# Optimization experiments

Measured on AMD Instinct MI355X. Metric: run time of the kernel, lower is better.

## Reference

```python
import jax, jax.numpy as jnp
import numpy as np

DIM = 768
HEADS = 12
HD = DIM // HEADS
L = 196
N = 128


def layernorm(x, g, b, eps=1e-5):
    x32 = x.astype(jnp.float32)
    mu = jnp.mean(x32, axis=-1, keepdims=True)
    var = jnp.mean(jnp.square(x32 - mu), axis=-1, keepdims=True)
    return ((x32 - mu) * jax.lax.rsqrt(var + eps) * g + b).astype(x.dtype)


def setup_inputs() -> dict:
    key = jax.random.key(0)
    ks = jax.random.split(key, 16)
    s_lin = 1.0 / np.sqrt(DIM)
    s_hd = 1.0 / np.sqrt(HD)
    return {
        "x": jax.random.normal(ks[0], (L, N, DIM), jnp.float32),
        "cls": jax.random.normal(ks[1], (1, N, DIM), jnp.float32),
        "g1": jnp.ones((DIM,), jnp.float32),
        "b1": jnp.zeros((DIM,), jnp.float32),
        "g2": jnp.ones((DIM,), jnp.float32),
        "b2": jnp.zeros((DIM,), jnp.float32),
        "Wq": jax.random.uniform(ks[2], (DIM, DIM), jnp.float32, -s_lin, s_lin),
        "Wk": jax.random.uniform(ks[3], (DIM, DIM), jnp.float32, -s_lin, s_lin),
        "Wv": jax.random.uniform(ks[4], (DIM, DIM), jnp.float32, -s_lin, s_lin),
        "p1_w1": jax.random.uniform(ks[5], (HD, HD), jnp.float32, -s_hd, s_hd),
        "p1_b1": jax.random.uniform(ks[6], (HD,), jnp.float32, -s_hd, s_hd),
        "p1_w2": jax.random.uniform(ks[7], (HD, HD), jnp.float32, -s_hd, s_hd),
        "p1_b2": jax.random.uniform(ks[8], (HD,), jnp.float32, -s_hd, s_hd),
        "fc_w": jax.random.uniform(ks[9], (DIM, DIM), jnp.float32, -s_lin, s_lin),
        "fc_b": jax.random.uniform(ks[10], (DIM,), jnp.float32, -s_lin, s_lin),
        "proj_w": jax.random.uniform(ks[11], (DIM, DIM), jnp.float32, -s_lin, s_lin),
        "proj_b": jax.random.uniform(ks[12], (DIM,), jnp.float32, -s_lin, s_lin),
    }


def reference(x, cls, g1, b1, g2, b2, Wq, Wk, Wv, p1_w1, p1_b1, p1_w2, p1_b2, fc_w, fc_b, proj_w, proj_b):
    scale = HD ** (-0.5)
    xx = layernorm(jnp.concatenate([cls, x], axis=0), g1, b1)  # [L+1, N, D]
    q0 = xx[:1]   # [1, N, D] (residual)
    kv = xx[1:]   # [L, N, D]
    # torch nn.Linear: y = x @ W.T; B=1 hard-wired, keys flattened to L*N tokens
    q = (q0 @ Wq.T).reshape(1, N, HEADS, HD).transpose(0, 2, 1, 3)        # [1,H,N,hd]
    k = (kv @ Wk.T).reshape(1, L * N, HEADS, HD).transpose(0, 2, 1, 3)    # [1,H,LN,hd]
    v = (kv @ Wv.T).reshape(1, L * N, HEADS, HD).transpose(0, 2, 1, 3)    # [1,H,LN,hd]
    scores = jnp.einsum('bhqd,bhkd->bhqk', q, k) * scale                  # [1,H,N,LN]
    attn = jax.nn.softmax(scores, axis=-1)
    # predictor gate: MLP -> mean over head_dim -> softmax over singleton axis (=1)
    temq = jnp.tanh(jax.nn.relu(q @ p1_w1.T + p1_b1) @ p1_w2.T + p1_b2)   # [1,H,N,hd]
    temq = jnp.mean(temq, axis=-1, keepdims=True)                          # [1,H,N,1]
    temq = jax.nn.softmax(temq, axis=-1)                                   # ones (faithful)
    attn = (temq - 0.5) * attn
    ctx = jnp.einsum('bhqk,bhkd->bhqd', attn, v)                           # [1,H,N,hd]
    ctx = ctx.transpose(0, 2, 1, 3).reshape(1, N, DIM)
    q1 = q0 + ctx
    h = layernorm(q1, g2, b2)
    m = h @ fc_w.T + fc_b
    m = m * jax.nn.sigmoid(1.702 * m)  # QuickGELU
    m = m @ proj_w.T + proj_b
    return q1 + m  # [1, N, D]
```

## Files before the change

kernel.cpp:

```cpp
#include <hip/hip_runtime.h>

#define DIM 768
#define HEADS 12
#define HD 64
#define NB 128
#define ROWS_ALL 25216
#define ROWS_KV  25088
#define NCHUNK 64

typedef __attribute__((ext_vector_type(8))) short short8;
typedef __attribute__((ext_vector_type(4))) short short4v;
typedef __attribute__((ext_vector_type(4))) float f32x4;
typedef __attribute__((ext_vector_type(4))) unsigned int uint4v;

__device__ __forceinline__ unsigned short f2bf(float f) {
  union { float f; unsigned u; } a; a.f = f;
  return (unsigned short)((a.u + 0x7fffu + ((a.u >> 16) & 1u)) >> 16);
}
__device__ __forceinline__ float bf2f(unsigned short u) {
  union { unsigned u; float f; } a; a.u = ((unsigned)u) << 16;
  return a.f;
}

__device__ __forceinline__ void gload16(const void* g, void* l) {
  __builtin_amdgcn_global_load_lds(
      (__attribute__((address_space(1))) void*)g,
      (__attribute__((address_space(3))) void*)l, 16, 0, 0);
}

__global__ __launch_bounds__(256) void ln1_cast(
    const float* __restrict__ x, const float* __restrict__ cls,
    const float* __restrict__ g, const float* __restrict__ b,
    unsigned short* __restrict__ xx, float* __restrict__ q0f,
    const float* __restrict__ Wq, const float* __restrict__ Wk,
    const float* __restrict__ Wv, const float* __restrict__ fcw,
    const float* __restrict__ pw, unsigned short* __restrict__ wpk)
{
  int blk = blockIdx.x, tid = threadIdx.x;
  if (blk < ROWS_ALL / 4) {
    int row = blk * 4 + (tid >> 6);
    int lane = tid & 63;
    const float* src = (row < NB) ? (cls + (size_t)row * DIM)
                                  : (x + (size_t)(row - NB) * DIM);
    float4 v[3];
    float s = 0.f;
#pragma unroll
    for (int i = 0; i < 3; ++i) {
      v[i] = ((const float4*)src)[lane + 64 * i];
      s += v[i].x + v[i].y + v[i].z + v[i].w;
    }
#pragma unroll
    for (int o = 32; o; o >>= 1) s += __shfl_xor(s, o);
    float mean = s * (1.f / 768.f);
    float ss = 0.f;
#pragma unroll
    for (int i = 0; i < 3; ++i) {
      float a0 = v[i].x - mean, a1 = v[i].y - mean, a2 = v[i].z - mean, a3 = v[i].w - mean;
      ss += a0 * a0 + a1 * a1 + a2 * a2 + a3 * a3;
    }
#pragma unroll
    for (int o = 32; o; o >>= 1) ss += __shfl_xor(ss, o);
    float rs = rsqrtf(ss * (1.f / 768.f) + 1e-5f);
#pragma unroll
    for (int i = 0; i < 3; ++i) {
      int c4 = lane + 64 * i;
      float4 gv = ((const float4*)g)[c4];
      float4 bv = ((const float4*)b)[c4];
      float o0 = (v[i].x - mean) * rs * gv.x + bv.x;
      float o1 = (v[i].y - mean) * rs * gv.y + bv.y;
      float o2 = (v[i].z - mean) * rs * gv.z + bv.z;
      float o3 = (v[i].w - mean) * rs * gv.w + bv.w;
      ushort4 u; u.x = f2bf(o0); u.y = f2bf(o1); u.z = f2bf(o2); u.w = f2bf(o3);
      ((ushort4*)(xx + (size_t)row * DIM))[c4] = u;
      if (row < NB) {
        float4 fo; fo.x = o0; fo.y = o1; fo.z = o2; fo.w = o3;
        ((float4*)(q0f + (size_t)row * DIM))[c4] = fo;
      }
    }
  } else {
    int idx = blk - ROWS_ALL / 4;
    int w = idx / 576;
    int j4 = (idx % 576) * 256 + tid;
    const float* s = (w == 0) ? Wq : (w == 1) ? Wk : (w == 2) ? Wv
                   : (w == 3) ? fcw : pw;
    float4 v = ((const float4*)s)[j4];
    ushort4 u; u.x = f2bf(v.x); u.y = f2bf(v.y); u.z = f2bf(v.z); u.w = f2bf(v.w);
    ((ushort4*)(wpk + (size_t)w * (DIM * DIM)))[j4] = u;
  }
}

__global__ __launch_bounds__(256, 4) void gemm_fused(
    const unsigned short* __restrict__ xxkv, const unsigned short* __restrict__ Wkb,
    unsigned short* __restrict__ Kbf,
    const unsigned short* __restrict__ Wvb, unsigned short* __restrict__ Vtb,
    const unsigned short* __restrict__ xxall, const unsigned short* __restrict__ Wqb,
    unsigned short* __restrict__ Qbf)
{
  __shared__ unsigned short Asm[128 * 32];
  __shared__ unsigned short Bsm[128 * 32];
  int tid = threadIdx.x, wid = tid >> 6, lane = tid & 63;
  int l15 = lane & 15, l4 = lane >> 4;

  int nwg = gridDim.x;
  int bid = blockIdx.x;
  int q8 = nwg >> 3, r8 = nwg & 7;
  int xcd = bid & 7, rank = bid >> 3;
  int swz = (xcd < r8 ? xcd * (q8 + 1) : r8 * (q8 + 1) + (xcd - r8) * q8) + rank;

  const unsigned short *A, *Bt;
  unsigned short* C;
  int N, row0, col0;
  const int K = DIM;
  if (swz < 1176) {
    A = xxkv; Bt = Wkb; C = Kbf; N = DIM;
    row0 = (swz / 6) * 128; col0 = (swz % 6) * 128;
  } else if (swz < 2352) {
    int inner = swz - 1176;
    A = Wvb; Bt = xxkv; C = Vtb; N = ROWS_KV;
    row0 = (inner % 6) * 128; col0 = (inner / 6) * 128;
  } else {
    int inner = swz - 2352;
    A = xxall; Bt = Wqb; C = Qbf; N = DIM;
    row0 = 0; col0 = inner * 128;
  }

  int srow = tid >> 2;
  int sq = tid & 3;
  int sb = sq ^ ((srow >> 1) & 3);
  const char* Ag = (const char*)A + (size_t)(row0 + srow) * K * 2 + sb * 16;
  const char* Bg = (const char*)Bt + (size_t)(col0 + srow) * K * 2 + sb * 16;
  size_t rstep64 = (size_t)64 * K * 2;

  f32x4 acc[4][4] = {};
  int wr = (wid >> 1) * 64, wc = (wid & 1) * 64;
  const int nk = K >> 5;
  for (int t = 0; t < nk; ++t) {
    {
      const char* a0 = Ag + (size_t)t * 64;
      const char* b0 = Bg + (size_t)t * 64;
      char* la = (char*)Asm + wid * 1024;
      char* lb = (char*)Bsm + wid * 1024;
      gload16(a0,           la);
      gload16(a0 + rstep64, la + 4096);
      gload16(b0,           lb);
      gload16(b0 + rstep64, lb + 4096);
    }
    asm volatile("s_waitcnt vmcnt(0)" ::: "memory");
    __builtin_amdgcn_s_barrier();
    asm volatile("" ::: "memory");
    short8 aF[4], bF[4];
#pragma unroll
    for (int m = 0; m < 4; ++m) {
      int row = wr + m * 16 + l15;
      aF[m] = *(const short8*)((const char*)Asm + row * 64 + ((l4 ^ ((row >> 1) & 3)) << 4));
    }
#pragma unroll
    for (int n = 0; n < 4; ++n) {
      int row = wc + n * 16 + l15;
      bF[n] = *(const short8*)((const char*)Bsm + row * 64 + ((l4 ^ ((row >> 1) & 3)) << 4));
    }
    __builtin_amdgcn_s_setprio(1);
#pragma unroll
    for (int m = 0; m < 4; ++m)
#pragma unroll
      for (int n = 0; n < 4; ++n)
        acc[m][n] = __builtin_amdgcn_mfma_f32_16x16x32_bf16(aF[m], bF[n], acc[m][n], 0, 0, 0);
    __builtin_amdgcn_s_setprio(0);
    asm volatile("" ::: "memory");
    __builtin_amdgcn_s_barrier();
    asm volatile("" ::: "memory");
  }
#pragma unroll
  for (int m = 0; m < 4; ++m)
#pragma unroll
    for (int n = 0; n < 4; ++n)
#pragma unroll
      for (int r = 0; r < 4; ++r) {
        int rr = row0 + wr + m * 16 + l4 * 4 + r;
        int cc = col0 + wc + n * 16 + l15;
        C[(size_t)rr * N + cc] = f2bf(acc[m][n][r]);
      }
}

template <int EPI>
__global__ __launch_bounds__(256, 2) void gemm_bt64(
    const unsigned short* __restrict__ A, const unsigned short* __restrict__ Bt,
    void* __restrict__ Cout, int M, int N, int K,
    const float* __restrict__ bias, const float* __restrict__ addsrc)
{
  __shared__ unsigned short Asm[2][128 * 64];
  __shared__ unsigned short Bsm[2][128 * 64];
  int tid = threadIdx.x, wid = tid >> 6, lane = tid & 63;
  int l15 = lane & 15, l4 = lane >> 4;
  int row0 = blockIdx.y * 128, col0 = blockIdx.x * 128;

  int srow = tid >> 3;
  int scol = ((tid & 7) ^ (srow & 7)) << 4;
  const char* Ag = (const char*)A + (size_t)(row0 + srow) * K * 2 + scol;
  const char* Bg = (const char*)Bt + (size_t)(col0 + srow) * K * 2 + scol;
  size_t rstep32 = (size_t)32 * K * 2;

#define STAGE(buf, kt) do {                                           \
    const char* a0 = Ag + (size_t)(kt) * 128;                         \
    const char* b0 = Bg + (size_t)(kt) * 128;                         \
    char* la = (char*)Asm[buf] + wid * 1024;                          \
    char* lb = (char*)Bsm[buf] + wid * 1024;                          \
    gload16(a0,                la);                                   \
    gload16(a0 + rstep32,      la + 4096);                            \
    gload16(a0 + 2 * rstep32,  la + 8192);                            \
    gload16(a0 + 3 * rstep32,  la + 12288);                           \
    gload16(b0,                lb);                                   \
    gload16(b0 + rstep32,      lb + 4096);                            \
    gload16(b0 + 2 * rstep32,  lb + 8192);                            \
    gload16(b0 + 3 * rstep32,  lb + 12288);                           \
  } while (0)

  f32x4 acc[4][4] = {};
  int wr = (wid >> 1) * 64, wc = (wid & 1) * 64;
  int nk = K >> 6;
  STAGE(0, 0);
  for (int t = 0; t < nk; ++t) {
    int cur = t & 1;
    if (t + 1 < nk) {
      STAGE(cur ^ 1, t + 1);
      asm volatile("s_waitcnt vmcnt(8)" ::: "memory");
    } else {
      asm volatile("s_waitcnt vmcnt(0)" ::: "memory");
    }
    __builtin_amdgcn_s_barrier();
    asm volatile("" ::: "memory");
    const char* Ab = (const char*)Asm[cur];
    const char* Bb = (const char*)Bsm[cur];
#pragma unroll
    for (int kk = 0; kk < 2; ++kk) {
      short8 aF[4], bF[4];
#pragma unroll
      for (int m = 0; m < 4; ++m) {
        int row = wr + m * 16 + l15;
        aF[m] = *(const short8*)(Ab + row * 128 + ((((kk << 2) | l4) ^ (row & 7)) << 4));
      }
#pragma unroll
      for (int n = 0; n < 4; ++n) {
        int row = wc + n * 16 + l15;
        bF[n] = *(const short8*)(Bb + row * 128 + ((((kk << 2) | l4) ^ (row & 7)) << 4));
      }
#pragma unroll
      for (int m = 0; m < 4; ++m)
#pragma unroll
        for (int n = 0; n < 4; ++n)
          acc[m][n] = __builtin_amdgcn_mfma_f32_16x16x32_bf16(aF[m], bF[n], acc[m][n], 0, 0, 0);
    }
    asm volatile("" ::: "memory");
    __builtin_amdgcn_s_barrier();
    asm volatile("" ::: "memory");
  }
#undef STAGE
#pragma unroll
  for (int m = 0; m < 4; ++m)
#pragma unroll
    for (int n = 0; n < 4; ++n)
#pragma unroll
      for (int r = 0; r < 4; ++r) {
        int rr = row0 + wr + m * 16 + l4 * 4 + r;
        int cc = col0 + wc + n * 16 + l15;
        float v = acc[m][n][r];
        if (EPI == 1) {
          v += bias[cc];
          v = v / (1.f + __expf(-1.702f * v));
          ((unsigned short*)Cout)[(size_t)rr * N + cc] = f2bf(v);
        } else {
          v += bias[cc] + addsrc[(size_t)rr * N + cc];
          ((float*)Cout)[(size_t)rr * N + cc] = v;
        }
      }
}

__global__ __launch_bounds__(256, 4) void attn_partial(
    const unsigned short* __restrict__ Qb, const unsigned short* __restrict__ Kb,
    const unsigned short* __restrict__ Vt,
    unsigned short* __restrict__ Op, float* __restrict__ lp)
{
  __shared__ unsigned short Klds[2][64 * 64];
  __shared__ unsigned short Vlds[2][64 * 64];
  int tid = threadIdx.x, wid = tid >> 6, lane = tid & 63;
  int l15 = lane & 15, l4 = lane >> 4;
  int head = blockIdx.x >> 6, chunk = blockIdx.x & 63;
  int t0 = (49 * chunk) >> 3;
  int nkt = ((49 * (chunk + 1)) >> 3) - t0;

  short8 bQ[2][2];
#pragma unroll
  for (int m = 0; m < 2; ++m)
#pragma unroll
    for (int kk = 0; kk < 2; ++kk) {
      int qrow = wid * 32 + m * 16 + l15;
      bQ[m][kk] = *(const short8*)(Qb + (size_t)qrow * DIM + head * HD + kk * 32 + l4 * 8);
    }
  f32x4 accO[2][4] = {};
  float lrun[2] = { 0.f, 0.f };

  int srow = tid >> 3;
  int sblk = (tid & 7) ^ (srow & 7);
  const char* Kg = (const char*)(Kb + (size_t)(t0 * 64 + srow) * DIM + head * HD) + sblk * 16;
  const char* Vg = (const char*)(Vt + (size_t)(head * HD + srow) * ROWS_KV + t0 * 64) + sblk * 16;

#define STAGEKV(buf, kt) do {                                         \
    const char* k0 = Kg + (size_t)(kt) * 64 * DIM * 2;                \
    const char* v0 = Vg + (size_t)(kt) * 128;                         \
    char* lk = (char*)Klds[buf] + wid * 1024;                         \
    char* lv = (char*)Vlds[buf] + wid * 1024;                         \
    gload16(k0,                        lk);                           \
    gload16(k0 + (size_t)32 * DIM * 2, lk + 4096);                    \
    gload16(v0,                        lv);                           \
    gload16(v0 + (size_t)32 * ROWS_KV * 2, lv + 4096);                \
  } while (0)

  const float SC = 0.125f * 1.4426950408889634f;

  STAGEKV(0, 0);
  for (int kt = 0; kt < nkt; ++kt) {
    int cur = kt & 1;
    if (kt + 1 < nkt) {
      STAGEKV(cur ^ 1, kt + 1);
      asm volatile("s_waitcnt vmcnt(4)" ::: "memory");
    } else {
      asm volatile("s_waitcnt vmcnt(0)" ::: "memory");
    }
    __builtin_amdgcn_s_barrier();
    asm volatile("" ::: "memory");

    f32x4 sc[4][2] = {};
    __builtin_amdgcn_s_setprio(1);
#pragma unroll
    for (int kk = 0; kk < 2; ++kk) {
      short8 aK[4];
#pragma unroll
      for (int n = 0; n < 4; ++n) {
        int krow = n * 16 + l15;
        int blk = ((kk << 2) | l4) ^ (krow & 7);
        aK[n] = *(const short8*)((const char*)Klds[cur] + krow * 128 + blk * 16);
      }
#pragma unroll
      for (int n = 0; n < 4; ++n)
#pragma unroll
        for (int m = 0; m < 2; ++m)
          sc[n][m] = __builtin_amdgcn_mfma_f32_16x16x32_bf16(aK[n], bQ[m][kk], sc[n][m], 0, 0, 0);
    }
    __builtin_amdgcn_s_setprio(0);

    short8 pB[2][2];
#pragma unroll
    for (int m = 0; m < 2; ++m) {
      float rsum = 0.f;
#pragma unroll
      for (int n = 0; n < 4; ++n)
#pragma unroll
        for (int r = 0; r < 4; ++r) {
          float p;
          asm("v_exp_f32 %0, %1" : "=v"(p) : "v"(sc[n][m][r] * SC));
          sc[n][m][r] = p;
          rsum += p;
        }
      rsum += __shfl_xor(rsum, 16);
      rsum += __shfl_xor(rsum, 32);
      lrun[m] += rsum;
#pragma unroll
      for (int kk2 = 0; kk2 < 2; ++kk2) {
        uint4v pw;
#pragma unroll
        for (int w = 0; w < 4; ++w) {
          int n = 2 * kk2 + (w >> 1);
          int r0 = (w & 1) * 2;
          unsigned int u;
          asm("v_cvt_pk_bf16_f32 %0, %1, %2"
              : "=v"(u) : "v"(sc[n][m][r0]), "v"(sc[n][m][r0 + 1]));
          pw[w] = u;
        }
        pB[m][kk2] = __builtin_bit_cast(short8, pw);
      }
    }

    __builtin_amdgcn_s_setprio(1);
#pragma unroll
    for (int kk2 = 0; kk2 < 2; ++kk2) {
      short8 aV[4];
#pragma unroll
      for (int nb = 0; nb < 4; ++nb) {
        int row = nb * 16 + l15;
        int blk1 = (kk2 << 2) | (l4 >> 1);
        int in1 = (l4 & 1) << 3;
        const char* vb = (const char*)Vlds[cur] + row * 128;
        short4v lo = *(const short4v*)(vb + (((blk1 ^ (row & 7)) << 4) | in1));
        short4v hi = *(const short4v*)(vb + ((((blk1 + 2) ^ (row & 7)) << 4) | in1));
        aV[nb] = __builtin_shufflevector(lo, hi, 0, 1, 2, 3, 4, 5, 6, 7);
      }
#pragma unroll
      for (int m = 0; m < 2; ++m)
#pragma unroll
        for (int nb = 0; nb < 4; ++nb)
          accO[m][nb] = __builtin_amdgcn_mfma_f32_16x16x32_bf16(aV[nb], pB[m][kk2], accO[m][nb], 0, 0, 0);
    }
    __builtin_amdgcn_s_setprio(0);
    asm volatile("" ::: "memory");
    __builtin_amdgcn_s_barrier();
    asm volatile("" ::: "memory");
  }
#undef STAGEKV
  size_t pb = (size_t)(head * NCHUNK + chunk) * 128;
#pragma unroll
  for (int m = 0; m < 2; ++m) {
    int q = wid * 32 + m * 16 + l15;
#pragma unroll
    for (int nb = 0; nb < 4; ++nb) {
      ushort4 o;
      o.x = f2bf(accO[m][nb][0]); o.y = f2bf(accO[m][nb][1]);
      o.z = f2bf(accO[m][nb][2]); o.w = f2bf(accO[m][nb][3]);
      *(ushort4*)(Op + (pb + q) * 64 + nb * 16 + l4 * 4) = o;
    }
    if (l4 == 0) {
      lp[pb + q] = lrun[m];
    }
  }
}

__device__ __forceinline__ float blk_sum256(float v, volatile float* red) {
  int tid = threadIdx.x;
#pragma unroll
  for (int o = 32; o; o >>= 1) v += __shfl_xor(v, o);
  __syncthreads();
  if ((tid & 63) == 0) red[tid >> 6] = v;
  __syncthreads();
  return red[0] + red[1] + red[2] + red[3];
}

__global__ __launch_bounds__(256) void combine_ln2(
    const unsigned short* __restrict__ Op, const float* __restrict__ lp,
    const float* __restrict__ q0f, const float* __restrict__ g2, const float* __restrict__ b2,
    float* __restrict__ q1, unsigned short* __restrict__ hb)
{
  int q = blockIdx.x, tid = threadIdx.x;
  __shared__ float lS[HEADS * NCHUNK];
  __shared__ float red[4];
  for (int i = tid; i < HEADS * NCHUNK; i += 256)
    lS[i] = lp[(size_t)i * 128 + q];
  __syncthreads();
  float vals[3];
#pragma unroll
  for (int ii = 0; ii < 3; ++ii) {
    int c = tid + ii * 256;
    int h = c >> 6, d = c & 63;
    float num = 0.f, den = 0.f;
    for (int cc = 0; cc < NCHUNK; ++cc) {
      den += lS[h * NCHUNK + cc];
      num += bf2f(Op[((size_t)(h * NCHUNK + cc) * 128 + q) * 64 + d]);
    }
    float ctx = 0.5f * num / den;
    float v = q0f[(size_t)q * DIM + c] + ctx;
    q1[(size_t)q * DIM + c] = v;
    vals[ii] = v;
  }
  float s = blk_sum256(vals[0] + vals[1] + vals[2], red);
  float mean = s * (1.f / 768.f);
  float d0 = vals[0] - mean, d1 = vals[1] - mean, d2 = vals[2] - mean;
  float ss = blk_sum256(d0 * d0 + d1 * d1 + d2 * d2, red);
  float rs = rsqrtf(ss * (1.f / 768.f) + 1e-5f);
#pragma unroll
  for (int ii = 0; ii < 3; ++ii) {
    int c = tid + ii * 256;
    hb[(size_t)q * DIM + c] = f2bf((vals[ii] - mean) * rs * g2[c] + b2[c]);
  }
}

extern "C" void kernel_launch(void* const* d_in, const int* in_sizes, int n_in,
                              void* d_out, int out_size, void* d_ws, size_t ws_size,
                              hipStream_t stream) {
  const float* x   = (const float*)d_in[0];
  const float* cls = (const float*)d_in[1];
  const float* g1  = (const float*)d_in[2];
  const float* b1  = (const float*)d_in[3];
  const float* g2  = (const float*)d_in[4];
  const float* b2  = (const float*)d_in[5];
  const float* Wq  = (const float*)d_in[6];
  const float* Wk  = (const float*)d_in[7];
  const float* Wv  = (const float*)d_in[8];
  const float* fcw = (const float*)d_in[13];
  const float* fcb = (const float*)d_in[14];
  const float* pw  = (const float*)d_in[15];
  const float* pb  = (const float*)d_in[16];

  char* ws = (char*)d_ws;
  size_t off = 0;
  auto alloc = [&](size_t bytes) {
    char* p = ws + off;
    off += (bytes + 255) & ~(size_t)255;
    return p;
  };
  unsigned short* xxb  = (unsigned short*)alloc((size_t)ROWS_ALL * DIM * 2);
  float*          q0f  = (float*)alloc((size_t)NB * DIM * 4);
  unsigned short* Kbf  = (unsigned short*)alloc((size_t)ROWS_KV * DIM * 2);
  unsigned short* Vtb  = (unsigned short*)alloc((size_t)DIM * ROWS_KV * 2);
  unsigned short* Qbf  = (unsigned short*)alloc((size_t)NB * DIM * 2);
  unsigned short* wpk  = (unsigned short*)alloc((size_t)5 * DIM * DIM * 2);
  unsigned short* Opar = (unsigned short*)alloc((size_t)HEADS * NCHUNK * 128 * 64 * 2);
  float*          lpar = (float*)alloc((size_t)HEADS * NCHUNK * 128 * 4);
  float*          q1   = (float*)alloc((size_t)NB * DIM * 4);
  unsigned short* hb   = (unsigned short*)alloc((size_t)NB * DIM * 2);
  unsigned short* m1b  = (unsigned short*)alloc((size_t)NB * DIM * 2);

  unsigned short* Wqb = wpk;
  unsigned short* Wkb = wpk + (size_t)1 * DIM * DIM;
  unsigned short* Wvb = wpk + (size_t)2 * DIM * DIM;
  unsigned short* fwb = wpk + (size_t)3 * DIM * DIM;
  unsigned short* pwb = wpk + (size_t)4 * DIM * DIM;

  ln1_cast<<<ROWS_ALL / 4 + 2880, 256, 0, stream>>>(
      x, cls, g1, b1, xxb, q0f, Wq, Wk, Wv, fcw, pw, wpk);

  gemm_fused<<<1176 + 1176 + 6, 256, 0, stream>>>(
      xxb + (size_t)NB * DIM, Wkb, Kbf, Wvb, Vtb, xxb, Wqb, Qbf);

  attn_partial<<<HEADS * NCHUNK, 256, 0, stream>>>(Qbf, Kbf, Vtb, Opar, lpar);
  combine_ln2<<<NB, 256, 0, stream>>>(Opar, lpar, q0f, g2, b2, q1, hb);

  gemm_bt64<1><<<dim3(DIM / 128, 1), 256, 0, stream>>>(
      hb, fwb, m1b, NB, DIM, DIM, fcb, nullptr);
  gemm_bt64<2><<<dim3(DIM / 128, 1), 256, 0, stream>>>(
      m1b, pwb, d_out, NB, DIM, DIM, pb, q1);
}
```

Baseline: 165.1 us.

## Double-buffer LDS tiles in fused QKV GEMM to overlap global loads with MFMA

Splits the A and B shared-memory tiles into two buffers and prefetches the next K-slice while the current one is consumed by MFMA, waiting only on the older loads with vmcnt(4). This hides global-to-LDS latency that was previously exposed every iteration. It doubles LDS use per block and lowers the launch-bounds occupancy hint from 4 to 3 blocks per CU, trading some latency hiding through occupancy for hiding through software pipelining.

```diff
diff --git a/kernel.cpp b/kernel.cpp
--- a/kernel.cpp
+++ b/kernel.cpp
@@ -89,15 +89,15 @@
   }
 }
 
-__global__ __launch_bounds__(256, 4) void gemm_fused(
+__global__ __launch_bounds__(256, 3) void gemm_fused(
     const unsigned short* __restrict__ xxkv, const unsigned short* __restrict__ Wkb,
     unsigned short* __restrict__ Kbf,
     const unsigned short* __restrict__ Wvb, unsigned short* __restrict__ Vtb,
     const unsigned short* __restrict__ xxall, const unsigned short* __restrict__ Wqb,
     unsigned short* __restrict__ Qbf)
 {
-  __shared__ unsigned short Asm[128 * 32];
-  __shared__ unsigned short Bsm[128 * 32];
+  __shared__ unsigned short Asm[2][128 * 32];
+  __shared__ unsigned short Bsm[2][128 * 32];
   int tid = threadIdx.x, wid = tid >> 6, lane = tid & 63;
   int l15 = lane & 15, l4 = lane >> 4;
 
@@ -131,33 +131,43 @@
   const char* Bg = (const char*)Bt + (size_t)(col0 + srow) * K * 2 + sb * 16;
   size_t rstep64 = (size_t)64 * K * 2;
 
+#define STAGEF(buf, kt) do {                                          \
+    const char* a0 = Ag + (size_t)(kt) * 64;                          \
+    const char* b0 = Bg + (size_t)(kt) * 64;                          \
+    char* la = (char*)Asm[buf] + wid * 1024;                          \
+    char* lb = (char*)Bsm[buf] + wid * 1024;                          \
+    gload16(a0,           la);                                        \
+    gload16(a0 + rstep64, la + 4096);                                 \
+    gload16(b0,           lb);                                        \
+    gload16(b0 + rstep64, lb + 4096);                                 \
+  } while (0)
+
   f32x4 acc[4][4] = {};
   int wr = (wid >> 1) * 64, wc = (wid & 1) * 64;
   const int nk = K >> 5;
+  STAGEF(0, 0);
   for (int t = 0; t < nk; ++t) {
-    {
-      const char* a0 = Ag + (size_t)t * 64;
-      const char* b0 = Bg + (size_t)t * 64;
-      char* la = (char*)Asm + wid * 1024;
-      char* lb = (char*)Bsm + wid * 1024;
-      gload16(a0,           la);
-      gload16(a0 + rstep64, la + 4096);
-      gload16(b0,           lb);
-      gload16(b0 + rstep64, lb + 4096);
-    }
-    asm volatile("s_waitcnt vmcnt(0)" ::: "memory");
+    int cur = t & 1;
+    if (t + 1 < nk) {
+      STAGEF(cur ^ 1, t + 1);
+      asm volatile("s_waitcnt vmcnt(4)" ::: "memory");
+    } else {
+      asm volatile("s_waitcnt vmcnt(0)" ::: "memory");
+    }
     __builtin_amdgcn_s_barrier();
     asm volatile("" ::: "memory");
+    const char* Ab = (const char*)Asm[cur];
+    const char* Bb = (const char*)Bsm[cur];
     short8 aF[4], bF[4];
 #pragma unroll
     for (int m = 0; m < 4; ++m) {
       int row = wr + m * 16 + l15;
-      aF[m] = *(const short8*)((const char*)Asm + row * 64 + ((l4 ^ ((row >> 1) & 3)) << 4));
+      aF[m] = *(const short8*)(Ab + row * 64 + ((l4 ^ ((row >> 1) & 3)) << 4));
     }
 #pragma unroll
     for (int n = 0; n < 4; ++n) {
       int row = wc + n * 16 + l15;
-      bF[n] = *(const short8*)((const char*)Bsm + row * 64 + ((l4 ^ ((row >> 1) & 3)) << 4));
+      bF[n] = *(const short8*)(Bb + row * 64 + ((l4 ^ ((row >> 1) & 3)) << 4));
     }
     __builtin_amdgcn_s_setprio(1);
 #pragma unroll
@@ -170,6 +180,7 @@
     __builtin_amdgcn_s_barrier();
     asm volatile("" ::: "memory");
   }
+#undef STAGEF
 #pragma unroll
   for (int m = 0; m < 4; ++m)
 #pragma unroll
```

Measured after the change: 166.3 us. No clear change (+0.8%).

## Rewrite K/V/Q projection GEMM with 256x256 tiles, 8 waves, double-buffered phases

Applied to the files above, without the earlier changes.

Replaces the 128x128 single-buffered K/V/Q projection GEMM with a 512-thread, 256x256-tile kernel. It double-buffers 64-wide K slices in 128KB of LDS and splits each K step into four barrier-separated MFMA quadrants, so fragment loads overlap with compute. The goal is more data reuse per global load and better latency hiding. It also moves the per-iteration barrier to the top of the loop in the two other GEMM and attention loops, dropping one barrier per iteration. The Q tile now covers 256 rows while only 128 exist, so it reads past xxall into the K rows and writes into an enlarged Qbf buffer. That wastes some work, and the 128KB of LDS limits occupancy to one block per CU.

```diff
diff --git a/kernel.cpp b/kernel.cpp
--- a/kernel.cpp
+++ b/kernel.cpp
@@ -89,15 +89,14 @@
   }
 }
 
-__global__ __launch_bounds__(256, 4) void gemm_fused(
+__global__ __launch_bounds__(512) void gemm8ph(
     const unsigned short* __restrict__ xxkv, const unsigned short* __restrict__ Wkb,
     unsigned short* __restrict__ Kbf,
     const unsigned short* __restrict__ Wvb, unsigned short* __restrict__ Vtb,
     const unsigned short* __restrict__ xxall, const unsigned short* __restrict__ Wqb,
     unsigned short* __restrict__ Qbf)
 {
-  __shared__ unsigned short Asm[128 * 32];
-  __shared__ unsigned short Bsm[128 * 32];
+  __shared__ char lds[2][65536];
   int tid = threadIdx.x, wid = tid >> 6, lane = tid & 63;
   int l15 = lane & 15, l4 = lane >> 4;
 
@@ -111,74 +110,127 @@
   unsigned short* C;
   int N, row0, col0;
   const int K = DIM;
-  if (swz < 1176) {
+  if (swz < 294) {
     A = xxkv; Bt = Wkb; C = Kbf; N = DIM;
-    row0 = (swz / 6) * 128; col0 = (swz % 6) * 128;
-  } else if (swz < 2352) {
-    int inner = swz - 1176;
+    row0 = (swz / 3) * 256; col0 = (swz % 3) * 256;
+  } else if (swz < 588) {
+    int inner = swz - 294;
     A = Wvb; Bt = xxkv; C = Vtb; N = ROWS_KV;
-    row0 = (inner % 6) * 128; col0 = (inner / 6) * 128;
+    row0 = (inner % 3) * 256; col0 = (inner / 3) * 256;
   } else {
-    int inner = swz - 2352;
     A = xxall; Bt = Wqb; C = Qbf; N = DIM;
-    row0 = 0; col0 = inner * 128;
-  }
-
-  int srow = tid >> 2;
-  int sq = tid & 3;
-  int sb = sq ^ ((srow >> 1) & 3);
-  const char* Ag = (const char*)A + (size_t)(row0 + srow) * K * 2 + sb * 16;
-  const char* Bg = (const char*)Bt + (size_t)(col0 + srow) * K * 2 + sb * 16;
-  size_t rstep64 = (size_t)64 * K * 2;
-
-  f32x4 acc[4][4] = {};
-  int wr = (wid >> 1) * 64, wc = (wid & 1) * 64;
-  const int nk = K >> 5;
-  for (int t = 0; t < nk; ++t) {
-    {
-      const char* a0 = Ag + (size_t)t * 64;
-      const char* b0 = Bg + (size_t)t * 64;
-      char* la = (char*)Asm + wid * 1024;
-      char* lb = (char*)Bsm + wid * 1024;
-      gload16(a0,           la);
-      gload16(a0 + rstep64, la + 4096);
-      gload16(b0,           lb);
-      gload16(b0 + rstep64, lb + 4096);
-    }
-    asm volatile("s_waitcnt vmcnt(0)" ::: "memory");
+    row0 = 0; col0 = (swz - 588) * 256;
+  }
+
+  int srow = tid >> 3;
+  int sb = (tid & 7) ^ (srow & 7);
+  const char* Ag0 = (const char*)A + (size_t)(row0 + srow) * K * 2 + sb * 16;
+  const char* Bg0 = (const char*)Bt + (size_t)(col0 + srow) * K * 2 + sb * 16;
+
+#define STAGE8(s, kt) do {                                            \
+    size_t ko = (size_t)(kt) * 128;                                   \
+    char* la = lds[s] + wid * 1024;                                   \
+    char* lb = lds[s] + 32768 + wid * 1024;                           \
+    gload16(Ag0 + ko,          la);                                   \
+    gload16(Ag0 + 98304 + ko,  la + 8192);                            \
+    gload16(Ag0 + 196608 + ko, la + 16384);                           \
+    gload16(Ag0 + 294912 + ko, la + 24576);                           \
+    gload16(Bg0 + ko,          lb);                                   \
+    gload16(Bg0 + 98304 + ko,  lb + 8192);                            \
+    gload16(Bg0 + 196608 + ko, lb + 16384);                           \
+    gload16(Bg0 + 294912 + ko, lb + 24576);                           \
+  } while (0)
+
+#define MFMA_Q(QM, QN, BF) do {                                       \
+    __builtin_amdgcn_s_setprio(1);                                    \
+    _Pragma("unroll")                                                 \
+    for (int m_ = 0; m_ < 4; ++m_)                                    \
+      _Pragma("unroll")                                               \
+      for (int nn_ = 0; nn_ < 2; ++nn_)                               \
+        _Pragma("unroll")                                             \
+        for (int kk_ = 0; kk_ < 2; ++kk_)                             \
+          acc[(QM)*4+m_][(QN)*2+nn_] =                                \
+            __builtin_amdgcn_mfma_f32_16x16x32_bf16(                  \
+              aF[m_][kk_], BF[nn_][kk_], acc[(QM)*4+m_][(QN)*2+nn_],  \
+              0, 0, 0);                                               \
+    __builtin_amdgcn_s_setprio(0);                                    \
+  } while (0)
+
+  f32x4 acc[8][4] = {};
+  int wr = (wid >> 2) * 128, wc = (wid & 3) * 64;
+  short8 aF[4][2], bF0[2][2], bF1[2][2];
+
+  STAGE8(0, 0);
+  const int nt = K >> 6;
+  for (int t = 0; t < nt; ++t) {
+    int cur = t & 1;
+    if (t + 1 < nt) {
+      STAGE8(cur ^ 1, t + 1);
+      asm volatile("s_waitcnt vmcnt(8)" ::: "memory");
+    } else {
+      asm volatile("s_waitcnt vmcnt(0)" ::: "memory");
+    }
     __builtin_amdgcn_s_barrier();
     asm volatile("" ::: "memory");
-    short8 aF[4], bF[4];
+    const char* ldsA = lds[cur];
+    const char* ldsB = lds[cur] + 32768;
+
 #pragma unroll
     for (int m = 0; m < 4; ++m) {
       int row = wr + m * 16 + l15;
-      aF[m] = *(const short8*)((const char*)Asm + row * 64 + ((l4 ^ ((row >> 1) & 3)) << 4));
-    }
-#pragma unroll
-    for (int n = 0; n < 4; ++n) {
-      int row = wc + n * 16 + l15;
-      bF[n] = *(const short8*)((const char*)Bsm + row * 64 + ((l4 ^ ((row >> 1) & 3)) << 4));
-    }
-    __builtin_amdgcn_s_setprio(1);
-#pragma unroll
-    for (int m = 0; m < 4; ++m)
-#pragma unroll
-      for (int n = 0; n < 4; ++n)
-        acc[m][n] = __builtin_amdgcn_mfma_f32_16x16x32_bf16(aF[m], bF[n], acc[m][n], 0, 0, 0);
-    __builtin_amdgcn_s_setprio(0);
+#pragma unroll
+      for (int kk = 0; kk < 2; ++kk)
+        aF[m][kk] = *(const short8*)(ldsA + row * 128 + ((((kk << 2) | l4) ^ (row & 7)) << 4));
+    }
+#pragma unroll
+    for (int nn = 0; nn < 2; ++nn) {
+      int row = wc + nn * 16 + l15;
+#pragma unroll
+      for (int kk = 0; kk < 2; ++kk)
+        bF0[nn][kk] = *(const short8*)(ldsB + row * 128 + ((((kk << 2) | l4) ^ (row & 7)) << 4));
+    }
+    __builtin_amdgcn_s_barrier();
+    MFMA_Q(0, 0, bF0);
+    __builtin_amdgcn_s_barrier();
+
+#pragma unroll
+    for (int nn = 0; nn < 2; ++nn) {
+      int row = wc + (2 + nn) * 16 + l15;
+#pragma unroll
+      for (int kk = 0; kk < 2; ++kk)
+        bF1[nn][kk] = *(const short8*)(ldsB + row * 128 + ((((kk << 2) | l4) ^ (row & 7)) << 4));
+    }
+    __builtin_amdgcn_s_barrier();
+    MFMA_Q(0, 1, bF1);
+    __builtin_amdgcn_s_barrier();
+
+#pragma unroll
+    for (int m = 0; m < 4; ++m) {
+      int row = wr + (4 + m) * 16 + l15;
+#pragma unroll
+      for (int kk = 0; kk < 2; ++kk)
+        aF[m][kk] = *(const short8*)(ldsA + row * 128 + ((((kk << 2) | l4) ^ (row & 7)) << 4));
+    }
+    __builtin_amdgcn_s_barrier();
+    MFMA_Q(1, 1, bF1);
+    __builtin_amdgcn_s_barrier();
+
+    MFMA_Q(1, 0, bF0);
+    __builtin_amdgcn_s_barrier();
     asm volatile("" ::: "memory");
-    __builtin_amdgcn_s_barrier();
-    asm volatile("" ::: "memory");
-  }
-#pragma unroll
-  for (int m = 0; m < 4; ++m)
+  }
+#undef STAGE8
+#undef MFMA_Q
+
+#pragma unroll
+  for (int mi = 0; mi < 8; ++mi)
 #pragma unroll
     for (int n = 0; n < 4; ++n)
 #pragma unroll
       for (int r = 0; r < 4; ++r) {
-        int rr = row0 + wr + m * 16 + l4 * 4 + r;
+        int rr = row0 + wr + mi * 16 + l4 * 4 + r;
         int cc = col0 + wc + n * 16 + l15;
-        C[(size_t)rr * N + cc] = f2bf(acc[m][n][r]);
+        C[(size_t)rr * N + cc] = f2bf(acc[mi][n][r]);
       }
 }
 
@@ -221,14 +273,14 @@
   STAGE(0, 0);
   for (int t = 0; t < nk; ++t) {
     int cur = t & 1;
+    __builtin_amdgcn_s_barrier();
+    asm volatile("" ::: "memory");
     if (t + 1 < nk) {
       STAGE(cur ^ 1, t + 1);
       asm volatile("s_waitcnt vmcnt(8)" ::: "memory");
     } else {
       asm volatile("s_waitcnt vmcnt(0)" ::: "memory");
     }
-    __builtin_amdgcn_s_barrier();
-    asm volatile("" ::: "memory");
     const char* Ab = (const char*)Asm[cur];
     const char* Bb = (const char*)Bsm[cur];
 #pragma unroll
@@ -250,8 +302,6 @@
         for (int n = 0; n < 4; ++n)
           acc[m][n] = __builtin_amdgcn_mfma_f32_16x16x32_bf16(aF[m], bF[n], acc[m][n], 0, 0, 0);
     }
-    asm volatile("" ::: "memory");
-    __builtin_amdgcn_s_barrier();
     asm volatile("" ::: "memory");
   }
 #undef STAGE
@@ -320,14 +370,14 @@
   STAGEKV(0, 0);
   for (int kt = 0; kt < nkt; ++kt) {
     int cur = kt & 1;
+    __builtin_amdgcn_s_barrier();
+    asm volatile("" ::: "memory");
     if (kt + 1 < nkt) {
       STAGEKV(cur ^ 1, kt + 1);
       asm volatile("s_waitcnt vmcnt(4)" ::: "memory");
     } else {
       asm volatile("s_waitcnt vmcnt(0)" ::: "memory");
     }
-    __builtin_amdgcn_s_barrier();
-    asm volatile("" ::: "memory");
 
     f32x4 sc[4][2] = {};
     __builtin_amdgcn_s_setprio(1);
@@ -401,8 +451,6 @@
           accO[m][nb] = __builtin_amdgcn_mfma_f32_16x16x32_bf16(aV[nb], pB[m][kk2], accO[m][nb], 0, 0, 0);
     }
     __builtin_amdgcn_s_setprio(0);
-    asm volatile("" ::: "memory");
-    __builtin_amdgcn_s_barrier();
     asm volatile("" ::: "memory");
   }
 #undef STAGEKV
@@ -499,7 +547,7 @@
   float*          q0f  = (float*)alloc((size_t)NB * DIM * 4);
   unsigned short* Kbf  = (unsigned short*)alloc((size_t)ROWS_KV * DIM * 2);
   unsigned short* Vtb  = (unsigned short*)alloc((size_t)DIM * ROWS_KV * 2);
-  unsigned short* Qbf  = (unsigned short*)alloc((size_t)NB * DIM * 2);
+  unsigned short* Qbf  = (unsigned short*)alloc((size_t)256 * DIM * 2);
   unsigned short* wpk  = (unsigned short*)alloc((size_t)5 * DIM * DIM * 2);
   unsigned short* Opar = (unsigned short*)alloc((size_t)HEADS * NCHUNK * 128 * 64 * 2);
   float*          lpar = (float*)alloc((size_t)HEADS * NCHUNK * 128 * 4);
@@ -516,7 +564,7 @@
   ln1_cast<<<ROWS_ALL / 4 + 2880, 256, 0, stream>>>(
       x, cls, g1, b1, xxb, q0f, Wq, Wk, Wv, fcw, pw, wpk);
 
-  gemm_fused<<<1176 + 1176 + 6, 256, 0, stream>>>(
+  gemm8ph<<<591, 512, 0, stream>>>(
       xxb + (size_t)NB * DIM, Wkb, Kbf, Wvb, Vtb, xxb, Wqb, Qbf);
 
   attn_partial<<<HEADS * NCHUNK, 256, 0, stream>>>(Qbf, Kbf, Vtb, Opar, lpar);
```

Measured after the change: 171.0 us. 1.04x slower.
